# Kernel optimization log

Measured on AMD Instinct MI355X. Metric: run time of the kernel, lower is better.

Reference implementation:

```python
import jax, jax.numpy as jnp
import numpy as np

INPUT_SIZE = 128
OUTPUT_SIZE = 128
P_NUM = 16
BATCH = 131072


def setup_inputs() -> dict:
    key = jax.random.key(0)
    k_x, k_c = jax.random.split(key)
    x = jax.random.normal(k_x, (BATCH, INPUT_SIZE), dtype=jnp.float32)
    coef = jax.random.normal(k_c, (OUTPUT_SIZE, INPUT_SIZE, P_NUM), dtype=jnp.float32) * 0.1
    tanh_range = jnp.array(1.0, dtype=jnp.float32)
    return {"x": x, "coef": coef, "tanh_range": tanh_range}


def reference(x, coef, tanh_range):
    # Original: values = tanh(x*t); out[b,o] = sum_i sum_p coef[o,i,p] * values[b,i]
    # Equivalent fused form: (sum_p coef) applied as a single GEMM.
    values = jnp.tanh(x * tanh_range)          # [B, I]
    w = jnp.sum(coef, axis=2)                  # [O, I]
    return jnp.einsum('bi,oi->bo', values, w)  # [B, O]
```

## Files before the change

### kernel.cpp

```cpp
#include <hip/hip_runtime.h>

#define BATCH 131072
#define IN 128
#define OUT 128
#define PNUM 16

typedef _Float16 f16x8 __attribute__((ext_vector_type(8)));
typedef float f32x4 __attribute__((ext_vector_type(4)));

__device__ __forceinline__ float tanh_fast(float v) {
    float e = __expf(2.0f * v);
    return 1.0f - 2.0f * __builtin_amdgcn_rcpf(e + 1.0f);
}

__global__ __launch_bounds__(256) void prep_w_kernel(const float* __restrict__ coef,
                                                     _Float16* __restrict__ w) {
    int t = blockIdx.x * blockDim.x + threadIdx.x;
    const float4* p = (const float4*)(coef + (size_t)t * PNUM);
    float4 a = p[0], b = p[1], c = p[2], d = p[3];
    float s = (a.x + a.y + a.z + a.w) + (b.x + b.y + b.z + b.w)
            + (c.x + c.y + c.z + c.w) + (d.x + d.y + d.z + d.w);
    w[t] = (_Float16)s;
}

__global__ __launch_bounds__(256) void gemm_tanh_kernel(const float* __restrict__ x,
                                                        const _Float16* __restrict__ w,
                                                        const float* __restrict__ trange,
                                                        float* __restrict__ out) {
    const float t = trange[0];
    const int lane = threadIdx.x & 63;
    const int wv   = threadIdx.x >> 6;
    const int m = lane & 15;
    const int q = lane >> 4;

    const size_t row_base = (size_t)blockIdx.x * 64 + (size_t)wv * 16;
    const float* xrow = x + (row_base + m) * IN;

    f32x4 acc[8];
#pragma unroll
    for (int nt = 0; nt < 8; ++nt) acc[nt] = (f32x4){0.f, 0.f, 0.f, 0.f};

#pragma unroll
    for (int ks = 0; ks < 4; ++ks) {
        const int k0 = ks * 32 + q * 8;
        float4 xa = *(const float4*)(xrow + k0);
        float4 xb = *(const float4*)(xrow + k0 + 4);
        f16x8 afrag;
        afrag[0] = (_Float16)tanh_fast(xa.x * t);
        afrag[1] = (_Float16)tanh_fast(xa.y * t);
        afrag[2] = (_Float16)tanh_fast(xa.z * t);
        afrag[3] = (_Float16)tanh_fast(xa.w * t);
        afrag[4] = (_Float16)tanh_fast(xb.x * t);
        afrag[5] = (_Float16)tanh_fast(xb.y * t);
        afrag[6] = (_Float16)tanh_fast(xb.z * t);
        afrag[7] = (_Float16)tanh_fast(xb.w * t);
#pragma unroll
        for (int nt = 0; nt < 8; ++nt) {
            f16x8 bfrag = *(const f16x8*)(w + (size_t)(nt * 16 + m) * IN + k0);
            acc[nt] = __builtin_amdgcn_mfma_f32_16x16x32_f16(afrag, bfrag, acc[nt], 0, 0, 0);
        }
    }

    float* orow = out + (row_base + q * 4) * OUT + m;
#pragma unroll
    for (int nt = 0; nt < 8; ++nt) {
#pragma unroll
        for (int r = 0; r < 4; ++r) {
            orow[(size_t)r * OUT + nt * 16] = acc[nt][r];
        }
    }
}

extern "C" void kernel_launch(void* const* d_in, const int* in_sizes, int n_in,
                              void* d_out, int out_size, void* d_ws, size_t ws_size,
                              hipStream_t stream) {
    const float* x    = (const float*)d_in[0];
    const float* coef = (const float*)d_in[1];
    const float* tr   = (const float*)d_in[2];
    float* out = (float*)d_out;
    _Float16* w = (_Float16*)d_ws;

    prep_w_kernel<<<(OUT * IN) / 256, 256, 0, stream>>>(coef, w);
    gemm_tanh_kernel<<<BATCH / 64, 256, 0, stream>>>(x, w, tr, out);
}
```

Baseline: 142.8 us.

## Stage W in padded LDS, prefetch x, and use 512-thread blocks

Each block of eight waves now copies the whole fp16 weight matrix into LDS with a padded pitch, so the B fragments come from shared memory instead of repeated global/L2 loads. All x loads for a wave are issued up front, before the LDS fill and barrier, so their latency overlaps with the weight copy. Blocks grow to 512 threads covering 128 rows, with a launch-bounds occupancy hint. The cost is about 34 KB of LDS per block, which limits resident blocks, plus a 32 KB weight copy and a barrier in every block.

Measured after the change: 119.5 us. 1.2x faster.

```diff
diff --git a/kernel.cpp b/kernel.cpp
--- a/kernel.cpp
+++ b/kernel.cpp
@@ -4,6 +4,7 @@
 #define IN 128
 #define OUT 128
 #define PNUM 16
+#define LDS_PITCH 136
 
 typedef _Float16 f16x8 __attribute__((ext_vector_type(8)));
 typedef float f32x4 __attribute__((ext_vector_type(4)));
@@ -23,18 +24,51 @@
     w[t] = (_Float16)s;
 }
 
-__global__ __launch_bounds__(256) void gemm_tanh_kernel(const float* __restrict__ x,
-                                                        const _Float16* __restrict__ w,
-                                                        const float* __restrict__ trange,
-                                                        float* __restrict__ out) {
+__global__ __launch_bounds__(512, 5) void gemm_tanh_kernel(const float* __restrict__ x,
+                                                           const _Float16* __restrict__ w,
+                                                           const float* __restrict__ trange,
+                                                           float* __restrict__ out) {
+    __shared__ _Float16 wlds[OUT * LDS_PITCH];
+
     const float t = trange[0];
-    const int lane = threadIdx.x & 63;
-    const int wv   = threadIdx.x >> 6;
+    const int tid  = threadIdx.x;
+    const int lane = tid & 63;
+    const int wv   = tid >> 6;
     const int m = lane & 15;
     const int q = lane >> 4;
 
-    const size_t row_base = (size_t)blockIdx.x * 64 + (size_t)wv * 16;
+    const size_t row_base = (size_t)blockIdx.x * 128 + (size_t)wv * 16;
     const float* xrow = x + (row_base + m) * IN;
+
+    float4 xv[8];
+#pragma unroll
+    for (int ks = 0; ks < 4; ++ks) {
+        xv[2 * ks]     = *(const float4*)(xrow + ks * 32 + q * 8);
+        xv[2 * ks + 1] = *(const float4*)(xrow + ks * 32 + q * 8 + 4);
+    }
+
+#pragma unroll
+    for (int i = 0; i < 4; ++i) {
+        int idx = (i * 512 + tid) * 8;
+        int r = idx >> 7;
+        int c = idx & 127;
+        *(f16x8*)&wlds[r * LDS_PITCH + c] = *(const f16x8*)(w + idx);
+    }
+    __syncthreads();
+
+    f16x8 af[4];
+#pragma unroll
+    for (int ks = 0; ks < 4; ++ks) {
+        float4 a = xv[2 * ks], b = xv[2 * ks + 1];
+        af[ks][0] = (_Float16)tanh_fast(a.x * t);
+        af[ks][1] = (_Float16)tanh_fast(a.y * t);
+        af[ks][2] = (_Float16)tanh_fast(a.z * t);
+        af[ks][3] = (_Float16)tanh_fast(a.w * t);
+        af[ks][4] = (_Float16)tanh_fast(b.x * t);
+        af[ks][5] = (_Float16)tanh_fast(b.y * t);
+        af[ks][6] = (_Float16)tanh_fast(b.z * t);
+        af[ks][7] = (_Float16)tanh_fast(b.w * t);
+    }
 
     f32x4 acc[8];
 #pragma unroll
@@ -42,22 +76,11 @@
 
 #pragma unroll
     for (int ks = 0; ks < 4; ++ks) {
-        const int k0 = ks * 32 + q * 8;
-        float4 xa = *(const float4*)(xrow + k0);
-        float4 xb = *(const float4*)(xrow + k0 + 4);
-        f16x8 afrag;
-        afrag[0] = (_Float16)tanh_fast(xa.x * t);
-        afrag[1] = (_Float16)tanh_fast(xa.y * t);
-        afrag[2] = (_Float16)tanh_fast(xa.z * t);
-        afrag[3] = (_Float16)tanh_fast(xa.w * t);
-        afrag[4] = (_Float16)tanh_fast(xb.x * t);
-        afrag[5] = (_Float16)tanh_fast(xb.y * t);
-        afrag[6] = (_Float16)tanh_fast(xb.z * t);
-        afrag[7] = (_Float16)tanh_fast(xb.w * t);
+        const int kb = ks * 32 + q * 8;
 #pragma unroll
         for (int nt = 0; nt < 8; ++nt) {
-            f16x8 bfrag = *(const f16x8*)(w + (size_t)(nt * 16 + m) * IN + k0);
-            acc[nt] = __builtin_amdgcn_mfma_f32_16x16x32_f16(afrag, bfrag, acc[nt], 0, 0, 0);
+            f16x8 bf = *(const f16x8*)&wlds[(nt * 16 + m) * LDS_PITCH + kb];
+            acc[nt] = __builtin_amdgcn_mfma_f32_16x16x32_f16(af[ks], bf, acc[nt], 0, 0, 0);
         }
     }
 
@@ -81,5 +104,5 @@
     _Float16* w = (_Float16*)d_ws;
 
     prep_w_kernel<<<(OUT * IN) / 256, 256, 0, stream>>>(coef, w);
-    gemm_tanh_kernel<<<BATCH / 64, 256, 0, stream>>>(x, w, tr, out);
+    gemm_tanh_kernel<<<BATCH / 128, 512, 0, stream>>>(x, w, tr, out);
 }
```
